# Kernel optimization log

Hardware: AMD Instinct MI355X
Metric: run time of the kernel (lower is better)

Reference implementation:

```python
import jax, jax.numpy as jnp
import numpy as np

SR = 48000
HARMONIC_NUM = 8          # -> 9 harmonics total
SINE_AMP = 0.1
NOISE_STD = 0.003
VOICED_THRESHOLD = 0.0
B, T, UPP = 8, 2000, 480
S = T * UPP


def setup_inputs() -> dict:
    key = jax.random.key(0)
    k_f0, k_mask, k_ri, k_noise = jax.random.split(key, 4)
    f0 = jax.random.uniform(k_f0, (B, 1, T), jnp.float32, 80.0, 500.0)
    voiced = (jax.random.uniform(k_mask, (B, 1, T)) > 0.2).astype(jnp.float32)
    f0 = f0 * voiced
    # random initial phases; harmonic 0 gets phase 0 (as in torch code)
    rand_ini = jax.random.uniform(k_ri, (B, HARMONIC_NUM + 1), jnp.float32)
    rand_ini = rand_ini.at[:, 0].set(0.0)
    noise_raw = jax.random.normal(k_noise, (B, S), jnp.float32)
    # linear mixing layer: weight = 1/(H+1), bias = 0 per nn.init in __init__
    w = jnp.full((HARMONIC_NUM + 1,), 1.0 / (HARMONIC_NUM + 1), jnp.float32)
    b = jnp.zeros((1,), jnp.float32)
    return {"f0": f0, "rand_ini": rand_ini, "noise_raw": noise_raw,
            "w": w, "b": b, "upp": UPP}


def reference(f0, rand_ini, noise_raw, w, b, upp):
    # f0: [B,1,T] Hz -> nearest-upsample to [B, S]
    f0u = jnp.repeat(f0[:, 0, :], upp, axis=1)              # [B, S]
    uv = (f0u > VOICED_THRESHOLD).astype(f0.dtype)          # [B, S]
    rad = f0u * (2.0 * np.pi / SR)
    # cumsum is linear: one cumsum, broadcast-multiply by harmonic index
    base_phase = jnp.cumsum(rad, axis=1)                    # [B, S]
    mult = jnp.arange(1, HARMONIC_NUM + 2, dtype=f0.dtype)  # [H+1]
    phase = base_phase[:, :, None] * mult + rand_ini[:, None, :] * (2.0 * np.pi)
    sines = jnp.sin(phase) * uv[:, :, None]                 # [B, S, H+1]
    har = jnp.tanh(sines @ w + b[0]) * SINE_AMP             # [B, S]
    noise = noise_raw * NOISE_STD                            # [B, S]
    return har[:, None, :], noise[:, None, :], uv[:, None, :]
```

## Files before the change

### kernel.cpp

```cpp
#include <hip/hip_runtime.h>
#include <hip/hip_bf16.h>
#include <math.h>

constexpr int   B_   = 8;
constexpr int   T_   = 2000;
constexpr int   UPP_ = 480;
constexpr int   S_   = T_ * UPP_;
constexpr int   NH   = 9;
constexpr int   QPR  = S_ / 4;
constexpr int   NQ   = B_ * QPR;
constexpr float INV_SR = 1.0f / 48000.0f;

__global__ __launch_bounds__(256) void frame_scan_kernel(
    const float* __restrict__ f0,
    float2* __restrict__ ftab)
{
    __shared__ double lds[256];
    const int b = blockIdx.x;
    const int j = threadIdx.x;
    constexpr int CH = 8;
    const int t0 = j * CH;

    float fc[CH];
    double local = 0.0;
    #pragma unroll
    for (int k = 0; k < CH; ++k) {
        int t = t0 + k;
        float v = (t < T_) ? f0[b * T_ + t] : 0.0f;
        fc[k] = v * INV_SR;
        local += (double)fc[k] * (double)UPP_;
    }

    lds[j] = local;
    __syncthreads();

    double x = local;
    #pragma unroll
    for (int off = 1; off < 256; off <<= 1) {
        double y = (j >= off) ? lds[j - off] : 0.0;
        __syncthreads();
        x += y;
        lds[j] = x;
        __syncthreads();
    }
    double excl = x - local;

    #pragma unroll
    for (int k = 0; k < CH; ++k) {
        int t = t0 + k;
        if (t < T_) {
            double ph = excl - floor(excl);
            ftab[b * T_ + t] = make_float2((float)ph, fc[k]);
            excl += (double)fc[k] * (double)UPP_;
        }
    }
}

__global__ __launch_bounds__(256) void synth_kernel(
    const float* __restrict__ rand_ini,
    const float* __restrict__ noise_raw,
    const float* __restrict__ w,
    const float* __restrict__ bb,
    const float2* __restrict__ ftab,
    float* __restrict__ out)
{
    int q = blockIdx.x * blockDim.x + threadIdx.x;
    if (q >= NQ) return;

    int b  = q / QPR;
    int r  = q - b * QPR;
    int s0 = r * 4;
    int t  = s0 / UPP_;
    int i0 = s0 - t * UPP_;

    float2 pf   = ftab[b * T_ + t];
    float  Pred = pf.x;
    float  fcyc = pf.y;
    float  uvf  = (fcyc > 0.0f) ? 1.0f : 0.0f;

    float wr[NH], ri[NH];
    #pragma unroll
    for (int h = 0; h < NH; ++h) {
        wr[h] = w[h];
        ri[h] = rand_ini[b * NH + h];
    }
    float bias = bb[0];

    const float4 nz = *(const float4*)(noise_raw + (size_t)q * 4);

    float har[4];
    #pragma unroll
    for (int k = 0; k < 4; ++k) {
        float base = Pred + fcyc * (float)(i0 + 1 + k);
        float acc = 0.0f;
        #pragma unroll
        for (int h = 0; h < NH; ++h) {
            float ph = base * (float)(h + 1) + ri[h];
            float fr = ph - floorf(ph);
#if __has_builtin(__builtin_amdgcn_sinf)
            float sv = __builtin_amdgcn_sinf(fr);
#else
            float sv = __sinf(fr * 6.2831853071795864769f);
#endif
            acc = fmaf(sv, wr[h], acc);
        }
        float xx = acc * uvf + bias;
        float e  = __expf(2.0f * xx);
        har[k]   = (e - 1.0f) / (e + 1.0f) * 0.1f;
    }

    float* harp = out;
    float* nzp  = out + (size_t)B_ * S_;
    float* uvp  = out + (size_t)2 * B_ * S_;

    *(float4*)(harp + (size_t)q * 4) = make_float4(har[0], har[1], har[2], har[3]);
    *(float4*)(nzp  + (size_t)q * 4) = make_float4(nz.x * 0.003f, nz.y * 0.003f,
                                                   nz.z * 0.003f, nz.w * 0.003f);
    *(float4*)(uvp  + (size_t)q * 4) = make_float4(uvf, uvf, uvf, uvf);
}

extern "C" void kernel_launch(void* const* d_in, const int* in_sizes, int n_in,
                              void* d_out, int out_size, void* d_ws, size_t ws_size,
                              hipStream_t stream) {
    const float* f0        = (const float*)d_in[0];
    const float* rand_ini  = (const float*)d_in[1];
    const float* noise_raw = (const float*)d_in[2];
    const float* w         = (const float*)d_in[3];
    const float* bb        = (const float*)d_in[4];

    float2* ftab = (float2*)d_ws;

    frame_scan_kernel<<<B_, 256, 0, stream>>>(f0, ftab);
    synth_kernel<<<(NQ + 255) / 256, 256, 0, stream>>>(
        rand_ini, noise_raw, w, bb, ftab, (float*)d_out);
}
```

Measured before the change: 30.35 us.

## Use wave-shuffle scan, 8 samples per thread, skip sines for unvoiced frames

The frame prefix scan now uses 64-lane shuffle scans and a small per-wave offset array instead of a 256-step LDS scan with repeated barriers. The synth kernel processes 8 samples per thread with two float4 accesses per stream, halving thread count and amortizing index math and parameter loads. Unvoiced frames take a branch that writes the constant tanh(bias) and skips the 9 sine evaluations. Divergence is low because an unvoiced frame covers 480 contiguous samples, but each thread now uses more registers and fewer waves are launched.

```diff
diff --git a/kernel.cpp b/kernel.cpp
--- a/kernel.cpp
+++ b/kernel.cpp
@@ -7,17 +7,20 @@
 constexpr int   UPP_ = 480;
 constexpr int   S_   = T_ * UPP_;
 constexpr int   NH   = 9;
-constexpr int   QPR  = S_ / 4;
-constexpr int   NQ   = B_ * QPR;
+constexpr int   SPT  = 8;
+constexpr int   TPR  = S_ / SPT;
+constexpr int   NT   = B_ * TPR;
 constexpr float INV_SR = 1.0f / 48000.0f;
 
 __global__ __launch_bounds__(256) void frame_scan_kernel(
     const float* __restrict__ f0,
     float2* __restrict__ ftab)
 {
-    __shared__ double lds[256];
-    const int b = blockIdx.x;
-    const int j = threadIdx.x;
+    __shared__ double wsum[4];
+    const int b    = blockIdx.x;
+    const int j    = threadIdx.x;
+    const int lane = j & 63;
+    const int wid  = j >> 6;
     constexpr int CH = 8;
     const int t0 = j * CH;
 
@@ -31,19 +34,21 @@
         local += (double)fc[k] * (double)UPP_;
     }
 
-    lds[j] = local;
+    double x = local;
+    #pragma unroll
+    for (int off = 1; off < 64; off <<= 1) {
+        double y = __shfl_up(x, off, 64);
+        if (lane >= off) x += y;
+    }
+    if (lane == 63) wsum[wid] = x;
     __syncthreads();
 
-    double x = local;
+    double woff = 0.0;
     #pragma unroll
-    for (int off = 1; off < 256; off <<= 1) {
-        double y = (j >= off) ? lds[j - off] : 0.0;
-        __syncthreads();
-        x += y;
-        lds[j] = x;
-        __syncthreads();
-    }
-    double excl = x - local;
+    for (int w = 0; w < 3; ++w)
+        if (w < wid) woff += wsum[w];
+
+    double excl = (x + woff) - local;
 
     #pragma unroll
     for (int k = 0; k < CH; ++k) {
@@ -64,12 +69,12 @@
     const float2* __restrict__ ftab,
     float* __restrict__ out)
 {
-    int q = blockIdx.x * blockDim.x + threadIdx.x;
-    if (q >= NQ) return;
+    int g = blockIdx.x * blockDim.x + threadIdx.x;
+    if (g >= NT) return;
 
-    int b  = q / QPR;
-    int r  = q - b * QPR;
-    int s0 = r * 4;
+    int b  = g / TPR;
+    int r  = g - b * TPR;
+    int s0 = r * SPT;
     int t  = s0 / UPP_;
     int i0 = s0 - t * UPP_;
 
@@ -77,46 +82,59 @@
     float  Pred = pf.x;
     float  fcyc = pf.y;
     float  uvf  = (fcyc > 0.0f) ? 1.0f : 0.0f;
+    float  bias = bb[0];
 
-    float wr[NH], ri[NH];
-    #pragma unroll
-    for (int h = 0; h < NH; ++h) {
-        wr[h] = w[h];
-        ri[h] = rand_ini[b * NH + h];
-    }
-    float bias = bb[0];
+    const size_t row = (size_t)b * S_ + s0;
+    const float4 nz0 = *(const float4*)(noise_raw + row);
+    const float4 nz1 = *(const float4*)(noise_raw + row + 4);
 
-    const float4 nz = *(const float4*)(noise_raw + (size_t)q * 4);
+    float har[SPT];
 
-    float har[4];
-    #pragma unroll
-    for (int k = 0; k < 4; ++k) {
-        float base = Pred + fcyc * (float)(i0 + 1 + k);
-        float acc = 0.0f;
+    if (uvf > 0.0f) {
+        float wr[NH], ri[NH];
         #pragma unroll
         for (int h = 0; h < NH; ++h) {
-            float ph = base * (float)(h + 1) + ri[h];
-            float fr = ph - floorf(ph);
+            wr[h] = w[h];
+            ri[h] = rand_ini[b * NH + h];
+        }
+        #pragma unroll
+        for (int k = 0; k < SPT; ++k) {
+            float base = Pred + fcyc * (float)(i0 + 1 + k);
+            float acc = 0.0f;
+            #pragma unroll
+            for (int h = 0; h < NH; ++h) {
+                float ph = base * (float)(h + 1) + ri[h];
+                float fr = ph - floorf(ph);
 #if __has_builtin(__builtin_amdgcn_sinf)
-            float sv = __builtin_amdgcn_sinf(fr);
+                float sv = __builtin_amdgcn_sinf(fr);
 #else
-            float sv = __sinf(fr * 6.2831853071795864769f);
+                float sv = __sinf(fr * 6.2831853071795864769f);
 #endif
-            acc = fmaf(sv, wr[h], acc);
+                acc = fmaf(sv, wr[h], acc);
+            }
+            float xx = acc + bias;
+            float e  = __expf(2.0f * xx);
+            har[k]   = (e - 1.0f) / (e + 1.0f) * 0.1f;
         }
-        float xx = acc * uvf + bias;
-        float e  = __expf(2.0f * xx);
-        har[k]   = (e - 1.0f) / (e + 1.0f) * 0.1f;
+    } else {
+        float e  = __expf(2.0f * bias);
+        float hv = (e - 1.0f) / (e + 1.0f) * 0.1f;
+        #pragma unroll
+        for (int k = 0; k < SPT; ++k) har[k] = hv;
     }
 
     float* harp = out;
     float* nzp  = out + (size_t)B_ * S_;
     float* uvp  = out + (size_t)2 * B_ * S_;
 
-    *(float4*)(harp + (size_t)q * 4) = make_float4(har[0], har[1], har[2], har[3]);
-    *(float4*)(nzp  + (size_t)q * 4) = make_float4(nz.x * 0.003f, nz.y * 0.003f,
-                                                   nz.z * 0.003f, nz.w * 0.003f);
-    *(float4*)(uvp  + (size_t)q * 4) = make_float4(uvf, uvf, uvf, uvf);
+    *(float4*)(harp + row)     = make_float4(har[0], har[1], har[2], har[3]);
+    *(float4*)(harp + row + 4) = make_float4(har[4], har[5], har[6], har[7]);
+    *(float4*)(nzp + row)      = make_float4(nz0.x * 0.003f, nz0.y * 0.003f,
+                                             nz0.z * 0.003f, nz0.w * 0.003f);
+    *(float4*)(nzp + row + 4)  = make_float4(nz1.x * 0.003f, nz1.y * 0.003f,
+                                             nz1.z * 0.003f, nz1.w * 0.003f);
+    *(float4*)(uvp + row)      = make_float4(uvf, uvf, uvf, uvf);
+    *(float4*)(uvp + row + 4)  = make_float4(uvf, uvf, uvf, uvf);
 }
 
 extern "C" void kernel_launch(void* const* d_in, const int* in_sizes, int n_in,
@@ -131,6 +149,6 @@
     float2* ftab = (float2*)d_ws;
 
     frame_scan_kernel<<<B_, 256, 0, stream>>>(f0, ftab);
-    synth_kernel<<<(NQ + 255) / 256, 256, 0, stream>>>(
+    synth_kernel<<<(NT + 255) / 256, 256, 0, stream>>>(
         rand_ini, noise_raw, w, bb, ftab, (float*)d_out);
 }
```

New measurement: 34.45 us. +13.5%, slower.
